# Optimization experiments

Hardware: AMD Instinct MI355X
Metric: run time of the kernel (lower is better)

The kernel has to match this reference:

```python
import jax, jax.numpy as jnp
import numpy as np

N_NODES = 100000
N_EDGES = 1600000
N_GRAPHS = 256
IN_FEATS = 64
H_FEATS = 128
GN_EPS = 1e-5


def setup_inputs() -> dict:
    key = jax.random.key(0)
    ks = jax.random.split(key, 8)
    inputs = jax.random.normal(ks[0], (N_NODES, IN_FEATS), dtype=jnp.float32)
    edge_index = jax.random.randint(ks[1], (2, N_EDGES), 0, N_NODES, dtype=jnp.int64)
    batch = jnp.sort(jax.random.randint(ks[2], (N_NODES,), 0, N_GRAPHS, dtype=jnp.int64))
    edge_attr = jax.random.normal(ks[3], (N_EDGES, 8), dtype=jnp.float32)
    W1 = jax.random.normal(ks[4], (IN_FEATS, H_FEATS), dtype=jnp.float32) * 0.05
    W2 = jax.random.normal(ks[5], (H_FEATS, H_FEATS), dtype=jnp.float32) * 0.05
    W3 = jax.random.normal(ks[6], (H_FEATS, H_FEATS), dtype=jnp.float32) * 0.05
    return {
        'inputs': inputs, 'edge_index': edge_index, 'batch': batch, 'edge_attr': edge_attr,
        'W1': W1, 'b1': jnp.zeros((H_FEATS,), jnp.float32),
        'W2': W2, 'b2': jnp.zeros((H_FEATS,), jnp.float32),
        'W3': W3, 'b3': jnp.zeros((H_FEATS,), jnp.float32),
        'gn_weight': jnp.ones((H_FEATS,), jnp.float32),
        'gn_bias': jnp.zeros((H_FEATS,), jnp.float32),
        'gn_mean_scale': jnp.ones((H_FEATS,), jnp.float32),
    }


def reference(inputs, edge_index, batch, edge_attr, W1, b1, W2, b2, W3, b3, gn_weight, gn_bias, gn_mean_scale):
    src, dst = edge_index[0], edge_index[1]
    # GINConv with eps=0: h_i = MLP((1+eps)*x_i + sum_{j in N(i)} x_j)
    agg = jax.ops.segment_sum(inputs[src], dst, num_segments=N_NODES)
    h = inputs + agg
    # 3-layer ReLU MLP
    h = jax.nn.relu(h @ W1 + b1)
    h = jax.nn.relu(h @ W2 + b2)
    h = jax.nn.relu(h @ W3 + b3)
    # GraphNorm (per-graph mean shift with learnable mean_scale, then per-graph rms normalize)
    cnt = jnp.maximum(jax.ops.segment_sum(jnp.ones((N_NODES, 1), h.dtype), batch, num_segments=N_GRAPHS), 1.0)
    mean = jax.ops.segment_sum(h, batch, num_segments=N_GRAPHS) / cnt  # [G, H]
    out = h - mean[batch] * gn_mean_scale
    var = jax.ops.segment_sum(out * out, batch, num_segments=N_GRAPHS) / cnt  # [G, H]
    h_emb = out / jnp.sqrt(var[batch] + GN_EPS) * gn_weight + gn_bias
    # add_residue=False -> plain ReLU
    h_emb = jax.nn.relu(h_emb)
    # global max pool over each graph segment
    flat = jax.ops.segment_max(h_emb, batch, num_segments=N_GRAPHS)
    return (h_emb, flat, edge_index, edge_attr, batch)
```

## Files before the change

### kernel.cpp

```cpp
#include <hip/hip_runtime.h>
#include <math.h>

#define N_NODES 100000
#define N_EDGES 1600000
#define N_GRAPHS 256
#define IN_F 64
#define H_F 128
#define GN_EPS 1e-5f
#define PAD 32
#define NBINS 8
#define LCAP 512
#define BINCAP (1 << 18)
#define NSUB 16
#define SUBW 782
#define SBCAP 16384
#define MG 782
#define CPB 1612
#define GCB 25000
#define GCPB 1000
#define CP_EI4 800000
#define CP_EIB 825000
#define EA_TOT4 3200000
#define WIN_LO 800000
#define WIN_HI 821504

typedef __attribute__((ext_vector_type(8))) short bf16x8;
typedef __attribute__((ext_vector_type(4))) float f32x4;

__device__ __forceinline__ float bf2f(unsigned short u) {
  return __uint_as_float(((unsigned int)u) << 16);
}
__device__ __forceinline__ unsigned short f2bf(float f) {
  unsigned int u = __float_as_uint(f);
  u += 0x7FFFu + ((u >> 16) & 1u);
  return (unsigned short)(u >> 16);
}
__device__ __forceinline__ int bsearch_batch(const int* __restrict__ batch, int target) {
  int lo = 0, hi = N_NODES;
  while (lo < hi) { int mid = (lo + hi) >> 1; if (batch[mid] < target) lo = mid + 1; else hi = mid; }
  return lo;
}

#define PREP_XH   1600000
#define PREP_GS   (PREP_XH + 16384)
#define PREP_WT   (PREP_GS + 40960)
#define PREP_CTR  (PREP_WT + 40)
#define PREP_FL   (PREP_CTR + 8192)
__global__ __launch_bounds__(256) void k_prep(
    const float4* __restrict__ xin, const float* __restrict__ W1,
    const float* __restrict__ W2, const float* __restrict__ W3,
    ushort4* __restrict__ xh4, float4* __restrict__ gsum4,
    unsigned short* __restrict__ wt, int4* __restrict__ ctr4,
    float4* __restrict__ flat4) {
  int i = blockIdx.x * 256 + threadIdx.x;
  if (i < PREP_XH) {
    float4 v = xin[i];
    ushort4 o;
    o.x = f2bf(v.x); o.y = f2bf(v.y); o.z = f2bf(v.z); o.w = f2bf(v.w);
    xh4[i] = o;
  } else if (i < PREP_GS) {
    gsum4[i - PREP_XH] = make_float4(0.f, 0.f, 0.f, 0.f);
  } else if (i < PREP_WT) {
    int j = i - PREP_GS;
    if (j < 8192) {
      int n = j >> 6, k = j & 63;
      wt[j] = f2bf(W1[(size_t)k * H_F + n]);
    } else if (j < 24576) {
      int jj = j - 8192;
      int n = jj >> 7, k = jj & 127;
      wt[j] = f2bf(W2[(size_t)k * H_F + n]);
    } else {
      int jj = j - 24576;
      int n = jj >> 7, k = jj & 127;
      wt[j] = f2bf(W3[(size_t)k * H_F + n]);
    }
  } else if (i < PREP_CTR) {
    ctr4[i - PREP_WT] = make_int4(0, 0, 0, 0);
  } else if (i < PREP_FL) {
    flat4[i - PREP_CTR] = make_float4(-INFINITY, -INFINITY, -INFINITY, -INFINITY);
  }
}

__global__ __launch_bounds__(256) void k_bin(
    const int* __restrict__ src, const int* __restrict__ dst,
    unsigned int* __restrict__ binBuf, int* __restrict__ gbc) {
  __shared__ unsigned int ebuf[NBINS][LCAP];
  __shared__ int lcnt[NBINS];
  __shared__ int lbase[NBINS];
  const int t = threadIdx.x;
  if (t < NBINS) lcnt[t] = 0;
  __syncthreads();
  for (int e0 = blockIdx.x * 256; e0 < N_EDGES; e0 += gridDim.x * 256) {
    int e = e0 + t;
    if (e < N_EDGES) {
      int s = src[e], d = dst[e];
      int b = d / 12500;
      int p = atomicAdd(&lcnt[b], 1);
      ebuf[b][p] = ((unsigned)(d - b * 12500) << 17) | (unsigned)s;
    }
    __syncthreads();
    if (t < NBINS && lcnt[t] >= 256) lbase[t] = atomicAdd(&gbc[t], lcnt[t]);
    __syncthreads();
#pragma unroll
    for (int b = 0; b < NBINS; ++b) {
      int c = lcnt[b];
      if (c >= 256) {
        unsigned int* gp = binBuf + (size_t)b * BINCAP + lbase[b];
        for (int i = t; i < c; i += 256) gp[i] = ebuf[b][i];
      }
    }
    __syncthreads();
    if (t < NBINS && lcnt[t] >= 256) lcnt[t] = 0;
    __syncthreads();
  }
  if (t < NBINS && lcnt[t] > 0) lbase[t] = atomicAdd(&gbc[t], lcnt[t]);
  __syncthreads();
#pragma unroll
  for (int b = 0; b < NBINS; ++b) {
    int c = lcnt[b];
    if (c > 0) {
      unsigned int* gp = binBuf + (size_t)b * BINCAP + lbase[b];
      for (int i = t; i < c; i += 256) gp[i] = ebuf[b][i];
    }
  }
}

__global__ __launch_bounds__(256) void k_bin2(
    const unsigned int* __restrict__ binBuf, const int* __restrict__ gbc,
    unsigned int* __restrict__ binBuf2, int* __restrict__ gbc2) {
  __shared__ unsigned int ebuf[NSUB][LCAP];
  __shared__ int lcnt[NSUB];
  __shared__ int lbase[NSUB];
  const int t = threadIdx.x;
  const int p = blockIdx.x & 7;
  const int blk = blockIdx.x >> 3;
  const int nb = gbc[p];
  const unsigned int* buf = binBuf + (size_t)p * BINCAP;
  if (t < NSUB) lcnt[t] = 0;
  __syncthreads();
  for (int i0 = blk * 256; i0 < nb; i0 += 32 * 256) {
    int i = i0 + t;
    if (i < nb) {
      unsigned int e = buf[i];
      int dloc = (int)(e >> 17);
      int sub = dloc / SUBW;
      int p2 = atomicAdd(&lcnt[sub], 1);
      ebuf[sub][p2] = ((unsigned)(dloc - sub * SUBW) << 17) | (e & 131071u);
    }
    __syncthreads();
    if (t < NSUB && lcnt[t] >= 256)
      lbase[t] = atomicAdd(&gbc2[p * NSUB + t], lcnt[t]);
    __syncthreads();
#pragma unroll
    for (int b = 0; b < NSUB; ++b) {
      int c = lcnt[b];
      if (c >= 256) {
        unsigned int* gp = binBuf2 + (size_t)(p * NSUB + b) * SBCAP + lbase[b];
        for (int i2 = t; i2 < c; i2 += 256) gp[i2] = ebuf[b][i2];
      }
    }
    __syncthreads();
    if (t < NSUB && lcnt[t] >= 256) lcnt[t] = 0;
    __syncthreads();
  }
  if (t < NSUB && lcnt[t] > 0)
    lbase[t] = atomicAdd(&gbc2[p * NSUB + t], lcnt[t]);
  __syncthreads();
#pragma unroll
  for (int b = 0; b < NSUB; ++b) {
    int c = lcnt[b];
    if (c > 0) {
      unsigned int* gp = binBuf2 + (size_t)(p * NSUB + b) * SBCAP + lbase[b];
      for (int i2 = t; i2 < c; i2 += 256) gp[i2] = ebuf[b][i2];
    }
  }
}

__global__ __launch_bounds__(256) void k_fill5(
    const unsigned int* __restrict__ binBuf2, const int* __restrict__ gbc2,
    int* __restrict__ csr, int* __restrict__ cnt,
    int* __restrict__ ovfc, int* __restrict__ ovf) {
  __shared__ int lcsr[SUBW * PAD];
  __shared__ int lcnt[SUBW];
  const int t = threadIdx.x;
  const int p = blockIdx.x & 7;
  const int sub = blockIdx.x >> 3;
  for (int j = t; j < SUBW; j += 256) lcnt[j] = 0;
  __syncthreads();
  const int n2 = gbc2[p * NSUB + sub];
  const unsigned int* buf = binBuf2 + (size_t)(p * NSUB + sub) * SBCAP;
  const int dbase = p * 12500 + sub * SUBW;
  for (int i = t; i < n2; i += 256) {
    unsigned int e = buf[i];
    int dloc2 = (int)(e >> 17);
    int s = (int)(e & 131071u);
    int pos = atomicAdd(&lcnt[dloc2], 1);
    if (pos < PAD) {
      lcsr[dloc2 * PAD + pos] = s;
    } else {
      int o = atomicAdd(ovfc, 1);
      ovf[2 * o] = s;
      ovf[2 * o + 1] = dbase + dloc2;
    }
  }
  __syncthreads();
  int rows = 12500 - sub * SUBW; if (rows > SUBW) rows = SUBW;
  int total4 = rows * (PAD / 4);
  int4* dst4 = (int4*)(csr + (size_t)dbase * PAD);
  const int4* src4 = (const int4*)lcsr;
  for (int i = t; i < total4; i += 256) dst4[i] = src4[i];
  for (int j = t; j < rows; j += 256)
    cnt[dbase + j] = lcnt[j];
}

__global__ __launch_bounds__(256) void k_gather(
    const unsigned short* __restrict__ xh, const int* __restrict__ csr,
    const int* __restrict__ cnt, unsigned short* __restrict__ xa,
    const int* __restrict__ ovfc, const int* __restrict__ ovf,
    const int4* __restrict__ ei4, const int4* __restrict__ bat4,
    float4* __restrict__ o_ei4, float4* __restrict__ o_b4) {
  if (blockIdx.x >= GCB) {
    int cb = blockIdx.x - GCB;
    int stride = (gridDim.x - GCB) * 256;
    for (int i = cb * 256 + threadIdx.x; i < CP_EIB; i += stride) {
      if (i < CP_EI4) {
        int4 v = ei4[i];
        o_ei4[i] = make_float4((float)v.x, (float)v.y, (float)v.z, (float)v.w);
      } else {
        int j = i - CP_EI4;
        int4 v = bat4[j];
        o_b4[j] = make_float4((float)v.x, (float)v.y, (float)v.z, (float)v.w);
      }
    }
    return;
  }
  int wid = (blockIdx.x * 256 + threadIdx.x) >> 6;
  if (wid >= N_NODES) return;
  const int lane = threadIdx.x & 63;
  const int g = lane >> 4;
  const int fl = lane & 15;
  int rawdeg = cnt[wid];
  int deg = rawdeg > PAD ? PAD : rawdeg;
  int myE = csr[(size_t)wid * PAD + (lane & 31)];
  float s0 = 0.f, s1 = 0.f, s2 = 0.f, s3 = 0.f;
  int j = g;
  for (; j + 12 < deg; j += 16) {
    int sA = __shfl(myE, j);
    int sB = __shfl(myE, j + 4);
    int sC = __shfl(myE, j + 8);
    int sD = __shfl(myE, j + 12);
    ushort4 a = *(const ushort4*)&xh[(size_t)sA * IN_F + fl * 4];
    ushort4 b = *(const ushort4*)&xh[(size_t)sB * IN_F + fl * 4];
    ushort4 c = *(const ushort4*)&xh[(size_t)sC * IN_F + fl * 4];
    ushort4 d = *(const ushort4*)&xh[(size_t)sD * IN_F + fl * 4];
    s0 += bf2f(a.x) + bf2f(b.x) + bf2f(c.x) + bf2f(d.x);
    s1 += bf2f(a.y) + bf2f(b.y) + bf2f(c.y) + bf2f(d.y);
    s2 += bf2f(a.z) + bf2f(b.z) + bf2f(c.z) + bf2f(d.z);
    s3 += bf2f(a.w) + bf2f(b.w) + bf2f(c.w) + bf2f(d.w);
  }
  for (; j < deg; j += 4) {
    int sA = __shfl(myE, j);
    ushort4 a = *(const ushort4*)&xh[(size_t)sA * IN_F + fl * 4];
    s0 += bf2f(a.x); s1 += bf2f(a.y); s2 += bf2f(a.z); s3 += bf2f(a.w);
  }
  if (rawdeg > PAD && g == 0) {
    int n = *ovfc;
    for (int o = 0; o < n; ++o) {
      if (ovf[2 * o + 1] == wid) {
        int s = ovf[2 * o];
        ushort4 a = *(const ushort4*)&xh[(size_t)s * IN_F + fl * 4];
        s0 += bf2f(a.x); s1 += bf2f(a.y); s2 += bf2f(a.z); s3 += bf2f(a.w);
      }
    }
  }
  s0 += __shfl_xor(s0, 16); s1 += __shfl_xor(s1, 16);
  s2 += __shfl_xor(s2, 16); s3 += __shfl_xor(s3, 16);
  s0 += __shfl_xor(s0, 32); s1 += __shfl_xor(s1, 32);
  s2 += __shfl_xor(s2, 32); s3 += __shfl_xor(s3, 32);
  if (g == 0) {
    ushort4 self = *(const ushort4*)&xh[(size_t)wid * IN_F + fl * 4];
    s0 += bf2f(self.x); s1 += bf2f(self.y);
    s2 += bf2f(self.z); s3 += bf2f(self.w);
    ushort4 r;
    r.x = f2bf(s0); r.y = f2bf(s1); r.z = f2bf(s2); r.w = f2bf(s3);
    *(ushort4*)&xa[(size_t)wid * IN_F + fl * 4] = r;
  }
}

__global__ __launch_bounds__(512) void k_mlp(
    const unsigned short* __restrict__ xa,
    const unsigned short* __restrict__ wt1,
    const unsigned short* __restrict__ wt2,
    const unsigned short* __restrict__ wt3,
    const float* __restrict__ b1, const float* __restrict__ b2,
    const float* __restrict__ b3,
    unsigned short* __restrict__ h3,
    const int* __restrict__ batch,
    float* __restrict__ gsum, float* __restrict__ gsumq,
    const int4* __restrict__ ei4, const int4* __restrict__ bat4,
    const float4* __restrict__ ea4,
    float4* __restrict__ o_ei4, float4* __restrict__ o_b4,
    float4* __restrict__ o_ea4, int eaMode) {
  __shared__ unsigned short sh[128 * 128];
  __shared__ float ssum[H_F], ssq[H_F];
  const int t = threadIdx.x;
  if (blockIdx.x >= MG) {
    int cb = blockIdx.x - MG;
    if (eaMode) {
      for (int i = cb * 512 + t; i < EA_TOT4; i += CPB * 512) {
        if (i >= WIN_LO && i < WIN_HI) continue;
        o_ea4[i] = ea4[i];
      }
    } else {
      for (int i = cb * 512 + t; i < CP_EIB; i += CPB * 512) {
        if (i < CP_EI4) {
          int4 v = ei4[i];
          o_ei4[i] = make_float4((float)v.x, (float)v.y, (float)v.z, (float)v.w);
        } else {
          int j = i - CP_EI4;
          int4 v = bat4[j];
          o_b4[j] = make_float4((float)v.x, (float)v.y, (float)v.z, (float)v.w);
        }
      }
    }
    return;
  }
  const int lane = t & 63;
  const int wv = t >> 6;
  const int row16 = lane & 15;
  const int kg = lane >> 4;
  const long blk0 = (long)blockIdx.x * 128;
  const int lr0 = (wv & 3) * 32;
  const int nb = (wv >> 2) * 4;
  f32x4 acc0[4], acc1[4];

  {
    long arow0 = blk0 + lr0 + row16;      if (arow0 > N_NODES - 1) arow0 = N_NODES - 1;
    long arow1 = blk0 + lr0 + 16 + row16; if (arow1 > N_NODES - 1) arow1 = N_NODES - 1;
    bf16x8 a0[2], a1[2];
    const unsigned short* ap0 = xa + arow0 * IN_F + kg * 8;
    const unsigned short* ap1 = xa + arow1 * IN_F + kg * 8;
#pragma unroll
    for (int s = 0; s < 2; ++s) {
      a0[s] = *(const bf16x8*)(ap0 + s * 32);
      a1[s] = *(const bf16x8*)(ap1 + s * 32);
    }
#pragma unroll
    for (int n = 0; n < 4; ++n) {
      acc0[n] = (f32x4){0.f, 0.f, 0.f, 0.f};
      acc1[n] = (f32x4){0.f, 0.f, 0.f, 0.f};
    }
#pragma unroll
    for (int n = 0; n < 4; ++n) {
      const unsigned short* wpn =
          wt1 + (size_t)((nb + n) * 16 + row16) * IN_F + kg * 8;
      bf16x8 b[2];
      b[0] = *(const bf16x8*)(wpn);
      b[1] = *(const bf16x8*)(wpn + 32);
      acc0[n] = __builtin_amdgcn_mfma_f32_16x16x32_bf16(a0[0], b[0], acc0[n], 0, 0, 0);
      acc0[n] = __builtin_amdgcn_mfma_f32_16x16x32_bf16(a0[1], b[1], acc0[n], 0, 0, 0);
      acc1[n] = __builtin_amdgcn_mfma_f32_16x16x32_bf16(a1[0], b[0], acc1[n], 0, 0, 0);
      acc1[n] = __builtin_amdgcn_mfma_f32_16x16x32_bf16(a1[1], b[1], acc1[n], 0, 0, 0);
    }
#pragma unroll
    for (int n = 0; n < 4; ++n) {
      int col = (nb + n) * 16 + row16;
      float bv = b1[col];
#pragma unroll
      for (int r = 0; r < 4; ++r) {
        int lrow0 = lr0 + kg * 4 + r;
        int lrow1 = lrow0 + 16;
        sh[lrow0 * 128 + (col ^ ((lrow0 & 7) << 3))] = f2bf(fmaxf(acc0[n][r] + bv, 0.f));
        sh[lrow1 * 128 + (col ^ ((lrow1 & 7) << 3))] = f2bf(fmaxf(acc1[n][r] + bv, 0.f));
      }
    }
  }
  __syncthreads();

  {
    const int lA0 = lr0 + row16, lA1 = lr0 + 16 + row16;
    bf16x8 a0[4], a1[4];
#pragma unroll
    for (int s = 0; s < 4; ++s) {
      int K0 = s * 32 + kg * 8;
      a0[s] = *(const bf16x8*)&sh[lA0 * 128 + (K0 ^ ((lA0 & 7) << 3))];
      a1[s] = *(const bf16x8*)&sh[lA1 * 128 + (K0 ^ ((lA1 & 7) << 3))];
    }
#pragma unroll
    for (int n = 0; n < 4; ++n) {
      acc0[n] = (f32x4){0.f, 0.f, 0.f, 0.f};
      acc1[n] = (f32x4){0.f, 0.f, 0.f, 0.f};
    }
#pragma unroll
    for (int n = 0; n < 4; ++n) {
      const unsigned short* wpn =
          wt2 + (size_t)((nb + n) * 16 + row16) * H_F + kg * 8;
      bf16x8 b[4];
#pragma unroll
      for (int s = 0; s < 4; ++s) b[s] = *(const bf16x8*)(wpn + s * 32);
#pragma unroll
      for (int s = 0; s < 4; ++s) {
        acc0[n] = __builtin_amdgcn_mfma_f32_16x16x32_bf16(a0[s], b[s], acc0[n], 0, 0, 0);
        acc1[n] = __builtin_amdgcn_mfma_f32_16x16x32_bf16(a1[s], b[s], acc1[n], 0, 0, 0);
      }
    }
    __syncthreads();
#pragma unroll
    for (int n = 0; n < 4; ++n) {
      int col = (nb + n) * 16 + row16;
      float bv = b2[col];
#pragma unroll
      for (int r = 0; r < 4; ++r) {
        int lrow0 = lr0 + kg * 4 + r;
        int lrow1 = lrow0 + 16;
        sh[lrow0 * 128 + (col ^ ((lrow0 & 7) << 3))] = f2bf(fmaxf(acc0[n][r] + bv, 0.f));
        sh[lrow1 * 128 + (col ^ ((lrow1 & 7) << 3))] = f2bf(fmaxf(acc1[n][r] + bv, 0.f));
      }
    }
  }
  __syncthreads();

  {
    const int lA0 = lr0 + row16, lA1 = lr0 + 16 + row16;
    bf16x8 a0[4], a1[4];
#pragma unroll
    for (int s = 0; s < 4; ++s) {
      int K0 = s * 32 + kg * 8;
      a0[s] = *(const bf16x8*)&sh[lA0 * 128 + (K0 ^ ((lA0 & 7) << 3))];
      a1[s] = *(const bf16x8*)&sh[lA1 * 128 + (K0 ^ ((lA1 & 7) << 3))];
    }
#pragma unroll
    for (int n = 0; n < 4; ++n) {
      acc0[n] = (f32x4){0.f, 0.f, 0.f, 0.f};
      acc1[n] = (f32x4){0.f, 0.f, 0.f, 0.f};
    }
#pragma unroll
    for (int n = 0; n < 4; ++n) {
      const unsigned short* wpn =
          wt3 + (size_t)((nb + n) * 16 + row16) * H_F + kg * 8;
      bf16x8 b[4];
#pragma unroll
      for (int s = 0; s < 4; ++s) b[s] = *(const bf16x8*)(wpn + s * 32);
#pragma unroll
      for (int s = 0; s < 4; ++s) {
        acc0[n] = __builtin_amdgcn_mfma_f32_16x16x32_bf16(a0[s], b[s], acc0[n], 0, 0, 0);
        acc1[n] = __builtin_amdgcn_mfma_f32_16x16x32_bf16(a1[s], b[s], acc1[n], 0, 0, 0);
      }
    }
#pragma unroll
    for (int n = 0; n < 4; ++n) {
      int col = (nb + n) * 16 + row16;
      float bv = b3[col];
#pragma unroll
      for (int r = 0; r < 4; ++r) {
        long row0 = blk0 + lr0 + kg * 4 + r;
        long row1 = row0 + 16;
        if (row0 < N_NODES)
          h3[row0 * H_F + col] = f2bf(fmaxf(acc0[n][r] + bv, 0.f));
        if (row1 < N_NODES)
          h3[row1 * H_F + col] = f2bf(fmaxf(acc1[n][r] + bv, 0.f));
      }
    }
    long lastrow = blk0 + 127; if (lastrow > N_NODES - 1) lastrow = N_NODES - 1;
    const int glo = batch[blk0];
    const int ghi = batch[lastrow];
    int br0[4], br1[4];
#pragma unroll
    for (int r = 0; r < 4; ++r) {
      long row0 = blk0 + lr0 + kg * 4 + r;
      long row1 = row0 + 16;
      br0[r] = (row0 < N_NODES) ? batch[row0] : -1;
      br1[r] = (row1 < N_NODES) ? batch[row1] : -1;
    }
    for (int g = glo; g <= ghi; ++g) {
      if (t < H_F) { ssum[t] = 0.f; ssq[t] = 0.f; }
      __syncthreads();
#pragma unroll
      for (int n = 0; n < 4; ++n) {
        int col = (nb + n) * 16 + row16;
        float bvn = b3[col];
        float sn = 0.f, qn = 0.f;
#pragma unroll
        for (int r = 0; r < 4; ++r) {
          if (br0[r] == g) { float f = fmaxf(acc0[n][r] + bvn, 0.f); sn += f; qn += f * f; }
          if (br1[r] == g) { float f = fmaxf(acc1[n][r] + bvn, 0.f); sn += f; qn += f * f; }
        }
        sn += __shfl_xor(sn, 16); qn += __shfl_xor(qn, 16);
        sn += __shfl_xor(sn, 32); qn += __shfl_xor(qn, 32);
        if (kg == 0) {
          atomicAdd(&ssum[col], sn);
          atomicAdd(&ssq[col], qn);
        }
      }
      __syncthreads();
      if (t < H_F) {
        unsafeAtomicAdd(&gsum[(size_t)g * H_F + t], ssum[t]);
        unsafeAtomicAdd(&gsumq[(size_t)g * H_F + t], ssq[t]);
      }
      __syncthreads();
    }
  }
}

__global__ __launch_bounds__(256) void k_apply2(
    const unsigned short* __restrict__ h3, const int* __restrict__ batch,
    const float* __restrict__ gsum, const float* __restrict__ gsumsq,
    const float* __restrict__ gms, const float* __restrict__ gw,
    const float* __restrict__ gb, float* __restrict__ hemb,
    float* __restrict__ flat) {
  const int t = threadIdx.x;
  const int rg = t >> 5, fq = t & 31;
  const int m0 = blockIdx.x * 32;
  const int r0 = m0 + rg * 4;
  const int c0 = fq * 4;
  const float4 bb = *(const float4*)&gb[c0];
  const float4 gm = *(const float4*)&gms[c0];
  const float4 gwv = *(const float4*)&gw[c0];
  const int glo = batch[m0], ghi = batch[m0 + 31];
  __shared__ int sb[2];
  __shared__ __align__(16) float4 mred[8][32];
  if (glo == ghi) {
    if (t < 2) sb[t] = bsearch_batch(batch, glo + t);
    __syncthreads();
    float c = fmaxf((float)(sb[1] - sb[0]), 1.0f);
    float4 S = *(const float4*)&gsum[(size_t)glo * H_F + c0];
    float4 Q = *(const float4*)&gsumsq[(size_t)glo * H_F + c0];
    float4 mm, ss;
    {
      float mean, ms, var;
      mean = S.x / c; ms = mean * gm.x; var = fmaxf(Q.x / c - 2.f * ms * mean + ms * ms, 0.f);
      mm.x = ms; ss.x = gwv.x * rsqrtf(var + GN_EPS);
      mean = S.y / c; ms = mean * gm.y; var = fmaxf(Q.y / c - 2.f * ms * mean + ms * ms, 0.f);
      mm.y = ms; ss.y = gwv.y * rsqrtf(var + GN_EPS);
      mean = S.z / c; ms = mean * gm.z; var = fmaxf(Q.z / c - 2.f * ms * mean + ms * ms, 0.f);
      mm.z = ms; ss.z = gwv.z * rsqrtf(var + GN_EPS);
      mean = S.w / c; ms = mean * gm.w; var = fmaxf(Q.w / c - 2.f * ms * mean + ms * ms, 0.f);
      mm.w = ms; ss.w = gwv.w * rsqrtf(var + GN_EPS);
    }
    float4 mx = {-INFINITY, -INFINITY, -INFINITY, -INFINITY};
#pragma unroll
    for (int i = 0; i < 4; ++i) {
      size_t idx = (size_t)(r0 + i) * H_F + c0;
      ushort4 u = *(const ushort4*)&h3[idx];
      float4 v;
      v.x = fmaxf((bf2f(u.x) - mm.x) * ss.x + bb.x, 0.f);
      v.y = fmaxf((bf2f(u.y) - mm.y) * ss.y + bb.y, 0.f);
      v.z = fmaxf((bf2f(u.z) - mm.z) * ss.z + bb.z, 0.f);
      v.w = fmaxf((bf2f(u.w) - mm.w) * ss.w + bb.w, 0.f);
      *(float4*)&hemb[idx] = v;
      mx.x = fmaxf(mx.x, v.x); mx.y = fmaxf(mx.y, v.y);
      mx.z = fmaxf(mx.z, v.z); mx.w = fmaxf(mx.w, v.w);
    }
    mred[rg][fq] = mx;
    __syncthreads();
    if (rg == 0) {
#pragma unroll
      for (int j = 1; j < 8; ++j) {
        float4 a = mred[j][fq];
        mx.x = fmaxf(mx.x, a.x); mx.y = fmaxf(mx.y, a.y);
        mx.z = fmaxf(mx.z, a.z); mx.w = fmaxf(mx.w, a.w);
      }
      int* pf = (int*)&flat[(size_t)glo * H_F + c0];
      atomicMax(pf + 0, __float_as_int(mx.x));
      atomicMax(pf + 1, __float_as_int(mx.y));
      atomicMax(pf + 2, __float_as_int(mx.z));
      atomicMax(pf + 3, __float_as_int(mx.w));
    }
  } else {
    int gcur = -1;
    float4 mm = {0,0,0,0}, ss = {0,0,0,0};
    float4 mx = {-INFINITY, -INFINITY, -INFINITY, -INFINITY};
#pragma unroll
    for (int i = 0; i < 4; ++i) {
      int g = batch[r0 + i];
      if (g != gcur) {
        if (gcur >= 0) {
          int* pf = (int*)&flat[(size_t)gcur * H_F + c0];
          atomicMax(pf + 0, __float_as_int(mx.x));
          atomicMax(pf + 1, __float_as_int(mx.y));
          atomicMax(pf + 2, __float_as_int(mx.z));
          atomicMax(pf + 3, __float_as_int(mx.w));
          mx = make_float4(-INFINITY, -INFINITY, -INFINITY, -INFINITY);
        }
        gcur = g;
        int lo = bsearch_batch(batch, g);
        int hi = bsearch_batch(batch, g + 1);
        float c = fmaxf((float)(hi - lo), 1.0f);
        float4 S = *(const float4*)&gsum[(size_t)g * H_F + c0];
        float4 Q = *(const float4*)&gsumsq[(size_t)g * H_F + c0];
        float mean, ms, var;
        mean = S.x / c; ms = mean * gm.x; var = fmaxf(Q.x / c - 2.f * ms * mean + ms * ms, 0.f);
        mm.x = ms; ss.x = gwv.x * rsqrtf(var + GN_EPS);
        mean = S.y / c; ms = mean * gm.y; var = fmaxf(Q.y / c - 2.f * ms * mean + ms * ms, 0.f);
        mm.y = ms; ss.y = gwv.y * rsqrtf(var + GN_EPS);
        mean = S.z / c; ms = mean * gm.z; var = fmaxf(Q.z / c - 2.f * ms * mean + ms * ms, 0.f);
        mm.z = ms; ss.z = gwv.z * rsqrtf(var + GN_EPS);
        mean = S.w / c; ms = mean * gm.w; var = fmaxf(Q.w / c - 2.f * ms * mean + ms * ms, 0.f);
        mm.w = ms; ss.w = gwv.w * rsqrtf(var + GN_EPS);
      }
      size_t idx = (size_t)(r0 + i) * H_F + c0;
      ushort4 u = *(const ushort4*)&h3[idx];
      float4 v;
      v.x = fmaxf((bf2f(u.x) - mm.x) * ss.x + bb.x, 0.f);
      v.y = fmaxf((bf2f(u.y) - mm.y) * ss.y + bb.y, 0.f);
      v.z = fmaxf((bf2f(u.z) - mm.z) * ss.z + bb.z, 0.f);
      v.w = fmaxf((bf2f(u.w) - mm.w) * ss.w + bb.w, 0.f);
      *(float4*)&hemb[idx] = v;
      mx.x = fmaxf(mx.x, v.x); mx.y = fmaxf(mx.y, v.y);
      mx.z = fmaxf(mx.z, v.z); mx.w = fmaxf(mx.w, v.w);
    }
    int* pf = (int*)&flat[(size_t)gcur * H_F + c0];
    atomicMax(pf + 0, __float_as_int(mx.x));
    atomicMax(pf + 1, __float_as_int(mx.y));
    atomicMax(pf + 2, __float_as_int(mx.z));
    atomicMax(pf + 3, __float_as_int(mx.w));
  }
}

__global__ __launch_bounds__(256) void k_copy_win(
    const float4* __restrict__ ea4, float4* __restrict__ o_ea4) {
  int i = WIN_LO + blockIdx.x * 256 + threadIdx.x;
  if (i < WIN_HI) o_ea4[i] = ea4[i];
}
__global__ __launch_bounds__(256) void k_copy_ea(
    const float4* __restrict__ ea4, float4* __restrict__ o_ea4, int n4) {
  int i = blockIdx.x * 256 + threadIdx.x;
  if (i < n4) o_ea4[i] = ea4[i];
}

extern "C" void kernel_launch(void* const* d_in, const int* in_sizes, int n_in,
                              void* d_out, int out_size, void* d_ws, size_t ws_size,
                              hipStream_t stream) {
  const float* inputs = (const float*)d_in[0];
  const int*   ei     = (const int*)d_in[1];
  const int*   batch  = (const int*)d_in[2];
  const float* eattr  = (const float*)d_in[3];
  const float* W1 = (const float*)d_in[4];
  const float* b1 = (const float*)d_in[5];
  const float* W2 = (const float*)d_in[6];
  const float* b2 = (const float*)d_in[7];
  const float* W3 = (const float*)d_in[8];
  const float* b3 = (const float*)d_in[9];
  const float* gw  = (const float*)d_in[10];
  const float* gb  = (const float*)d_in[11];
  const float* gms = (const float*)d_in[12];

  float* out = (float*)d_out;
  float* hemb  = out;
  float* flat  = out + 12800000;
  float* o_ei  = out + 12832768;
  float* o_ea  = out + 16032768;
  float* o_b   = out + 28832768;

  unsigned int*   binBuf  = (unsigned int*)hemb;
  unsigned int*   binBuf2 = (unsigned int*)(hemb + 2100000);
  unsigned short* xh = (unsigned short*)(hemb + 4200000);
  unsigned short* xa = (unsigned short*)(hemb + 7600000);
  int*            csr = (int*)o_ea;
  float* gsum  = o_ea + 3200000;
  float* gsumq = o_ea + 3232768;
  unsigned short* wt  = (unsigned short*)(o_ea + 3265536);
  unsigned short* wt1 = wt;
  unsigned short* wt2 = wt + 8192;
  unsigned short* wt3 = wt + 24576;

  const bool big = ws_size >= (size_t)25600000;
  unsigned short* h3;
  int *cnt, *ovfc, *gbc, *gbc2, *ovf;
  if (big) {
    h3   = (unsigned short*)d_ws;
    cnt  = (int*)o_ea + 3400000;
    ovfc = (int*)o_ea + 3500000;
    gbc  = ovfc + 8;
    gbc2 = ovfc + 16;
    ovf  = ovfc + 160;
  } else {
    h3   = (unsigned short*)(o_ea + 6400000);
    cnt  = (int*)o_ei;
    ovfc = (int*)o_ei + 100000;
    gbc  = ovfc + 8;
    gbc2 = ovfc + 16;
    ovf  = ovfc + 160;
  }

  k_prep<<<(PREP_FL + 255) / 256, 256, 0, stream>>>(
      (const float4*)inputs, W1, W2, W3, (ushort4*)xh, (float4*)gsum, wt,
      (int4*)ovfc, (float4*)flat);
  k_bin<<<512, 256, 0, stream>>>(ei, ei + N_EDGES, binBuf, gbc);
  k_bin2<<<256, 256, 0, stream>>>(binBuf, gbc, binBuf2, gbc2);
  k_fill5<<<NBINS * NSUB, 256, 0, stream>>>(binBuf2, gbc2, csr, cnt, ovfc, ovf);
  if (big) {
    k_gather<<<GCB + GCPB, 256, 0, stream>>>(xh, csr, cnt, xa, ovfc, ovf,
        (const int4*)ei, (const int4*)batch, (float4*)o_ei, (float4*)o_b);
    k_mlp<<<MG + CPB, 512, 0, stream>>>(xa, wt1, wt2, wt3, b1, b2, b3, h3, batch,
        gsum, gsumq, (const int4*)ei, (const int4*)batch, (const float4*)eattr,
        (float4*)o_ei, (float4*)o_b, (float4*)o_ea, 1);
    k_apply2<<<N_NODES / 32, 256, 0, stream>>>(h3, batch, gsum, gsumq, gms, gw, gb,
                                               hemb, flat);
    k_copy_win<<<(WIN_HI - WIN_LO + 255) / 256, 256, 0, stream>>>(
        (const float4*)eattr, (float4*)o_ea);
  } else {
    k_gather<<<GCB, 256, 0, stream>>>(xh, csr, cnt, xa, ovfc, ovf,
        (const int4*)ei, (const int4*)batch, (float4*)o_ei, (float4*)o_b);
    k_mlp<<<MG + CPB, 512, 0, stream>>>(xa, wt1, wt2, wt3, b1, b2, b3, h3, batch,
        gsum, gsumq, (const int4*)ei, (const int4*)batch, (const float4*)eattr,
        (float4*)o_ei, (float4*)o_b, (float4*)o_ea, 0);
    k_apply2<<<N_NODES / 32, 256, 0, stream>>>(h3, batch, gsum, gsumq, gms, gw, gb,
                                               hemb, flat);
    k_copy_ea<<<(N_EDGES * 2 + 255) / 256, 256, 0, stream>>>(
        (const float4*)eattr, (float4*)o_ea, N_EDGES * 2);
  }
}
```

Measured before the change: 234.1 us.

## Merge prep into binning kernel, move scratch to workspace, drop window copy

```diff
diff --git a/kernel.cpp b/kernel.cpp
--- a/kernel.cpp
+++ b/kernel.cpp
@@ -23,6 +23,7 @@
 #define EA_TOT4 3200000
 #define WIN_LO 800000
 #define WIN_HI 821504
+#define BINB 512
 
 typedef __attribute__((ext_vector_type(8))) short bf16x8;
 typedef __attribute__((ext_vector_type(4))) float f32x4;
@@ -44,53 +45,49 @@
 #define PREP_XH   1600000
 #define PREP_GS   (PREP_XH + 16384)
 #define PREP_WT   (PREP_GS + 40960)
-#define PREP_CTR  (PREP_WT + 40)
-#define PREP_FL   (PREP_CTR + 8192)
-__global__ __launch_bounds__(256) void k_prep(
+#define PREP_FL   (PREP_WT + 8192)
+__global__ __launch_bounds__(256) void k_binprep(
+    const int* __restrict__ src, const int* __restrict__ dst,
+    unsigned int* __restrict__ binBuf, int* __restrict__ gbc,
     const float4* __restrict__ xin, const float* __restrict__ W1,
     const float* __restrict__ W2, const float* __restrict__ W3,
     ushort4* __restrict__ xh4, float4* __restrict__ gsum4,
-    unsigned short* __restrict__ wt, int4* __restrict__ ctr4,
-    float4* __restrict__ flat4) {
-  int i = blockIdx.x * 256 + threadIdx.x;
-  if (i < PREP_XH) {
-    float4 v = xin[i];
-    ushort4 o;
-    o.x = f2bf(v.x); o.y = f2bf(v.y); o.z = f2bf(v.z); o.w = f2bf(v.w);
-    xh4[i] = o;
-  } else if (i < PREP_GS) {
-    gsum4[i - PREP_XH] = make_float4(0.f, 0.f, 0.f, 0.f);
-  } else if (i < PREP_WT) {
-    int j = i - PREP_GS;
-    if (j < 8192) {
-      int n = j >> 6, k = j & 63;
-      wt[j] = f2bf(W1[(size_t)k * H_F + n]);
-    } else if (j < 24576) {
-      int jj = j - 8192;
-      int n = jj >> 7, k = jj & 127;
-      wt[j] = f2bf(W2[(size_t)k * H_F + n]);
-    } else {
-      int jj = j - 24576;
-      int n = jj >> 7, k = jj & 127;
-      wt[j] = f2bf(W3[(size_t)k * H_F + n]);
-    }
-  } else if (i < PREP_CTR) {
-    ctr4[i - PREP_WT] = make_int4(0, 0, 0, 0);
-  } else if (i < PREP_FL) {
-    flat4[i - PREP_CTR] = make_float4(-INFINITY, -INFINITY, -INFINITY, -INFINITY);
-  }
-}
-
-__global__ __launch_bounds__(256) void k_bin(
-    const int* __restrict__ src, const int* __restrict__ dst,
-    unsigned int* __restrict__ binBuf, int* __restrict__ gbc) {
+    unsigned short* __restrict__ wt, float4* __restrict__ flat4) {
+  const int t = threadIdx.x;
+  if (blockIdx.x >= BINB) {
+    int i = (blockIdx.x - BINB) * 256 + t;
+    if (i < PREP_XH) {
+      float4 v = xin[i];
+      ushort4 o;
+      o.x = f2bf(v.x); o.y = f2bf(v.y); o.z = f2bf(v.z); o.w = f2bf(v.w);
+      xh4[i] = o;
+    } else if (i < PREP_GS) {
+      gsum4[i - PREP_XH] = make_float4(0.f, 0.f, 0.f, 0.f);
+    } else if (i < PREP_WT) {
+      int j = i - PREP_GS;
+      if (j < 8192) {
+        int n = j >> 6, k = j & 63;
+        wt[j] = f2bf(W1[(size_t)k * H_F + n]);
+      } else if (j < 24576) {
+        int jj = j - 8192;
+        int n = jj >> 7, k = jj & 127;
+        wt[j] = f2bf(W2[(size_t)k * H_F + n]);
+      } else {
+        int jj = j - 24576;
+        int n = jj >> 7, k = jj & 127;
+        wt[j] = f2bf(W3[(size_t)k * H_F + n]);
+      }
+    } else if (i < PREP_FL) {
+      flat4[i - PREP_WT] = make_float4(-INFINITY, -INFINITY, -INFINITY, -INFINITY);
+    }
+    return;
+  }
   __shared__ unsigned int ebuf[NBINS][LCAP];
   __shared__ int lcnt[NBINS];
   __shared__ int lbase[NBINS];
-  const int t = threadIdx.x;
   if (t < NBINS) lcnt[t] = 0;
   __syncthreads();
-  for (int e0 = blockIdx.x * 256; e0 < N_EDGES; e0 += gridDim.x * 256) {
+  for (int e0 = blockIdx.x * 256; e0 < N_EDGES; e0 += BINB * 256) {
     int e = e0 + t;
     if (e < N_EDGES) {
       int s = src[e], d = dst[e];
@@ -307,10 +304,8 @@
   if (blockIdx.x >= MG) {
     int cb = blockIdx.x - MG;
     if (eaMode) {
-      for (int i = cb * 512 + t; i < EA_TOT4; i += CPB * 512) {
-        if (i >= WIN_LO && i < WIN_HI) continue;
+      for (int i = cb * 512 + t; i < EA_TOT4; i += CPB * 512)
         o_ea4[i] = ea4[i];
-      }
     } else {
       for (int i = cb * 512 + t; i < CP_EIB; i += CPB * 512) {
         if (i < CP_EI4) {
@@ -333,6 +328,7 @@
   const int lr0 = (wv & 3) * 32;
   const int nb = (wv >> 2) * 4;
   f32x4 acc0[4], acc1[4];
+  bf16x8 w2p[4][4];
 
   {
     long arow0 = blk0 + lr0 + row16;      if (arow0 > N_NODES - 1) arow0 = N_NODES - 1;
@@ -344,6 +340,13 @@
     for (int s = 0; s < 2; ++s) {
       a0[s] = *(const bf16x8*)(ap0 + s * 32);
       a1[s] = *(const bf16x8*)(ap1 + s * 32);
+    }
+#pragma unroll
+    for (int n = 0; n < 4; ++n) {
+      const unsigned short* wpn =
+          wt2 + (size_t)((nb + n) * 16 + row16) * H_F + kg * 8;
+#pragma unroll
+      for (int s = 0; s < 4; ++s) w2p[n][s] = *(const bf16x8*)(wpn + s * 32);
     }
 #pragma unroll
     for (int n = 0; n < 4; ++n) {
@@ -393,15 +396,10 @@
     }
 #pragma unroll
     for (int n = 0; n < 4; ++n) {
-      const unsigned short* wpn =
-          wt2 + (size_t)((nb + n) * 16 + row16) * H_F + kg * 8;
-      bf16x8 b[4];
-#pragma unroll
-      for (int s = 0; s < 4; ++s) b[s] = *(const bf16x8*)(wpn + s * 32);
 #pragma unroll
       for (int s = 0; s < 4; ++s) {
-        acc0[n] = __builtin_amdgcn_mfma_f32_16x16x32_bf16(a0[s], b[s], acc0[n], 0, 0, 0);
-        acc1[n] = __builtin_amdgcn_mfma_f32_16x16x32_bf16(a1[s], b[s], acc1[n], 0, 0, 0);
+        acc0[n] = __builtin_amdgcn_mfma_f32_16x16x32_bf16(a0[s], w2p[n][s], acc0[n], 0, 0, 0);
+        acc1[n] = __builtin_amdgcn_mfma_f32_16x16x32_bf16(a1[s], w2p[n][s], acc1[n], 0, 0, 0);
       }
     }
     __syncthreads();
@@ -617,11 +615,6 @@
   }
 }
 
-__global__ __launch_bounds__(256) void k_copy_win(
-    const float4* __restrict__ ea4, float4* __restrict__ o_ea4) {
-  int i = WIN_LO + blockIdx.x * 256 + threadIdx.x;
-  if (i < WIN_HI) o_ea4[i] = ea4[i];
-}
 __global__ __launch_bounds__(256) void k_copy_ea(
     const float4* __restrict__ ea4, float4* __restrict__ o_ea4, int n4) {
   int i = blockIdx.x * 256 + threadIdx.x;
@@ -657,36 +650,40 @@
   unsigned short* xh = (unsigned short*)(hemb + 4200000);
   unsigned short* xa = (unsigned short*)(hemb + 7600000);
   int*            csr = (int*)o_ea;
-  float* gsum  = o_ea + 3200000;
-  float* gsumq = o_ea + 3232768;
-  unsigned short* wt  = (unsigned short*)(o_ea + 3265536);
+
+  const bool big = ws_size >= (size_t)25944064;
+  unsigned short* h3;
+  float *gsum, *gsumq;
+  unsigned short *wt;
+  int *cnt, *ovfc, *gbc, *gbc2, *ovf;
+  if (big) {
+    float* ws = (float*)d_ws;
+    h3    = (unsigned short*)d_ws;
+    gsum  = ws + 6400000;
+    gsumq = ws + 6432768;
+    wt    = (unsigned short*)(ws + 6465536);
+    cnt   = (int*)o_ea + 3400000;
+    ovfc  = (int*)o_ea + 3500000;
+  } else {
+    h3    = (unsigned short*)(o_ea + 6400000);
+    gsum  = o_ea + 3200000;
+    gsumq = o_ea + 3232768;
+    wt    = (unsigned short*)(o_ea + 3265536);
+    cnt   = (int*)o_ei;
+    ovfc  = (int*)o_ei + 100000;
+  }
+  gbc  = ovfc + 8;
+  gbc2 = ovfc + 16;
+  ovf  = ovfc + 160;
   unsigned short* wt1 = wt;
   unsigned short* wt2 = wt + 8192;
   unsigned short* wt3 = wt + 24576;
 
-  const bool big = ws_size >= (size_t)25600000;
-  unsigned short* h3;
-  int *cnt, *ovfc, *gbc, *gbc2, *ovf;
-  if (big) {
-    h3   = (unsigned short*)d_ws;
-    cnt  = (int*)o_ea + 3400000;
-    ovfc = (int*)o_ea + 3500000;
-    gbc  = ovfc + 8;
-    gbc2 = ovfc + 16;
-    ovf  = ovfc + 160;
-  } else {
-    h3   = (unsigned short*)(o_ea + 6400000);
-    cnt  = (int*)o_ei;
-    ovfc = (int*)o_ei + 100000;
-    gbc  = ovfc + 8;
-    gbc2 = ovfc + 16;
-    ovf  = ovfc + 160;
-  }
-
-  k_prep<<<(PREP_FL + 255) / 256, 256, 0, stream>>>(
-      (const float4*)inputs, W1, W2, W3, (ushort4*)xh, (float4*)gsum, wt,
-      (int4*)ovfc, (float4*)flat);
-  k_bin<<<512, 256, 0, stream>>>(ei, ei + N_EDGES, binBuf, gbc);
+  hipMemsetAsync(ovfc, 0, 160 * sizeof(int), stream);
+  const int prepBlocks = (PREP_FL + 255) / 256;
+  k_binprep<<<BINB + prepBlocks, 256, 0, stream>>>(
+      ei, ei + N_EDGES, binBuf, gbc, (const float4*)inputs, W1, W2, W3,
+      (ushort4*)xh, (float4*)gsum, wt, (float4*)flat);
   k_bin2<<<256, 256, 0, stream>>>(binBuf, gbc, binBuf2, gbc2);
   k_fill5<<<NBINS * NSUB, 256, 0, stream>>>(binBuf2, gbc2, csr, cnt, ovfc, ovf);
   if (big) {
@@ -697,8 +694,6 @@
         (float4*)o_ei, (float4*)o_b, (float4*)o_ea, 1);
     k_apply2<<<N_NODES / 32, 256, 0, stream>>>(h3, batch, gsum, gsumq, gms, gw, gb,
                                                hemb, flat);
-    k_copy_win<<<(WIN_HI - WIN_LO + 255) / 256, 256, 0, stream>>>(
-        (const float4*)eattr, (float4*)o_ea);
   } else {
     k_gather<<<GCB, 256, 0, stream>>>(xh, csr, cnt, xa, ovfc, ovf,
         (const int4*)ei, (const int4*)batch, (float4*)o_ei, (float4*)o_b);
```

Result: slower. 241.6 us (+3.2%).
